# Kernel tuning notes

Measured on AMD Instinct MI355X. Metric: run time of the kernel, lower is better.

The kernel has to match this reference:

```python
import jax, jax.numpy as jnp
import numpy as np

N, E, F, H = 50000, 500000, 128, 128   # nodes, edges, in-features, hidden
L, R, B = 3, 8, 30                     # layers, relations, bases
G, C = 16, 8                           # graphs in batch, classes
EPS = 1e-5


def setup_inputs() -> dict:
    key = jax.random.key(0)
    ks = jax.random.split(key, 16)
    x = jax.random.normal(ks[0], (N, F), jnp.float32)
    edge_index = jax.random.randint(ks[1], (2, E), 0, N)
    edge_attr = jax.random.randint(ks[2], (E,), 0, R)
    batch = jnp.sort(jax.random.randint(ks[3], (N,), 0, G))
    # RGCN params (all layers share shapes since F == H)
    basis = jax.random.normal(ks[4], (L, B, H, H), jnp.float32) * 0.05
    comp = jax.random.normal(ks[5], (L, R, B), jnp.float32) * 0.2
    root = jax.random.normal(ks[6], (L, H, H), jnp.float32) * 0.05
    bias = jnp.zeros((L, H), jnp.float32)
    # BatchNorm (eval mode: running stats)
    bn1_gamma = jnp.ones((F,), jnp.float32)
    bn1_beta = jnp.zeros((F,), jnp.float32)
    bn1_mean = jax.random.normal(ks[7], (F,), jnp.float32) * 0.1
    bn1_var = jax.random.uniform(ks[8], (F,), jnp.float32, 0.5, 1.5)
    bn2_gamma = jnp.ones((H,), jnp.float32)
    bn2_beta = jnp.zeros((H,), jnp.float32)
    bn2_mean = jax.random.normal(ks[9], (H,), jnp.float32) * 0.1
    bn2_var = jax.random.uniform(ks[10], (H,), jnp.float32, 0.5, 1.5)
    fc1_w = jax.random.normal(ks[11], (H, H), jnp.float32) * 0.05
    fc1_b = jnp.zeros((H,), jnp.float32)
    fc2_w = jax.random.normal(ks[12], (H, C), jnp.float32) * 0.05
    fc2_b = jnp.zeros((C,), jnp.float32)
    return dict(x=x, edge_index=edge_index, edge_attr=edge_attr, batch=batch,
                bn1_gamma=bn1_gamma, bn1_beta=bn1_beta, bn1_mean=bn1_mean, bn1_var=bn1_var,
                basis=basis, comp=comp, root=root, bias=bias,
                bn2_gamma=bn2_gamma, bn2_beta=bn2_beta, bn2_mean=bn2_mean, bn2_var=bn2_var,
                fc1_w=fc1_w, fc1_b=fc1_b, fc2_w=fc2_w, fc2_b=fc2_b)


def _bn(x, gamma, beta, mean, var):
    return (x - mean) * jax.lax.rsqrt(var + EPS) * gamma + beta


def _rgcn_layer(x, basis_l, comp_l, root_l, bias_l, src, dst, edge_attr):
    # root transform + bias
    out = x @ root_l + bias_l
    # relation-wise basis-decomposed message passing, mean-aggregated per relation
    for r in range(R):
        W_r = jnp.einsum('b,bio->io', comp_l[r], basis_l)  # [H, H]
        xw = x @ W_r                                       # [N, H]
        mask = (edge_attr == r).astype(x.dtype)            # [E]
        msg = xw[src] * mask[:, None]                      # gather + mask
        agg = jax.ops.segment_sum(msg, dst, num_segments=N)
        deg = jax.ops.segment_sum(mask, dst, num_segments=N)
        out = out + agg / jnp.maximum(deg, 1.0)[:, None]
    return out


def reference(x, edge_index, edge_attr, batch,
              bn1_gamma, bn1_beta, bn1_mean, bn1_var,
              basis, comp, root, bias,
              bn2_gamma, bn2_beta, bn2_mean, bn2_var,
              fc1_w, fc1_b, fc2_w, fc2_b):
    src, dst = edge_index[0], edge_index[1]
    h = _bn(x, bn1_gamma, bn1_beta, bn1_mean, bn1_var)
    for l in range(L):
        h = jax.nn.relu(_rgcn_layer(h, basis[l], comp[l], root[l], bias[l], src, dst, edge_attr))
        # dropout is identity in eval mode
    # global mean pool per graph
    sums = jax.ops.segment_sum(h, batch, num_segments=G)            # [G, H]
    counts = jax.ops.segment_sum(jnp.ones((N,), h.dtype), batch, num_segments=G)
    g = sums / jnp.maximum(counts, 1.0)[:, None]
    g = _bn(g, bn2_gamma, bn2_beta, bn2_mean, bn2_var)
    # temporal_type == 'mean'
    v = jax.nn.relu(g.mean(axis=0))                                 # [H]
    v = jax.nn.relu(v @ fc1_w + fc1_b)
    logits = v @ fc2_w + fc2_b                                      # [C]
    return jax.nn.log_softmax(logits, axis=-1)
```

## Files before the change

### kernel.cpp

```cpp
#include <hip/hip_runtime.h>
#include <hip/hip_bf16.h>

#define NN 50000
#define NE 500000
#define HID 128
#define LAYERS 3
#define RELS 8
#define BASES 30
#define GRAPHS 16
#define CLASSES 8
#define EPSV 1e-5f
#define NOUT (HID * (RELS + 1))
#define SCAN_CHUNK 1024
#define SCAN_NBLK ((NN + SCAN_CHUNK - 1) / SCAN_CHUNK)
#define PCHUNK 128

typedef __attribute__((ext_vector_type(8))) short short8;
typedef __attribute__((ext_vector_type(4))) float f32x4;
typedef __attribute__((ext_vector_type(2))) float f32x2;

__device__ __forceinline__ float bf2f(unsigned short u) {
    union { unsigned int i; float f; } x; x.i = ((unsigned int)u) << 16; return x.f;
}
__device__ __forceinline__ unsigned short f2bf(float f) {
    __hip_bfloat16 b = __float2bfloat16(f);
    return *(unsigned short*)&b;
}
__device__ __forceinline__ unsigned char f2fp8(float a) {
    return (unsigned char)(__builtin_amdgcn_cvt_pk_fp8_f32(a, a, 0, false) & 0xFF);
}
__device__ __forceinline__ f32x2 fp8x2_2f(unsigned short u) {
    return __builtin_amdgcn_cvt_pk_f32_fp8((int)u, false);
}

__global__ __launch_bounds__(256) void build_wcat(const float* __restrict__ basis,
                                                  const float* __restrict__ comp,
                                                  const float* __restrict__ root,
                                                  unsigned short* __restrict__ wT) {
    int bid = blockIdx.x;
    int l = bid >> 6;
    int k0 = (bid & 63) << 1;
    __shared__ float cl[RELS * BASES];
    int tid = threadIdx.x;
    if (tid < RELS * BASES) cl[tid] = comp[l * RELS * BASES + tid];
    __syncthreads();
    int j = tid & 127;
    int k = k0 + (tid >> 7);
    const float* bp = basis + ((size_t)l * BASES * HID + k) * HID + j;
    float acc[RELS];
#pragma unroll
    for (int r = 0; r < RELS; ++r) acc[r] = 0.f;
    for (int b = 0; b < BASES; ++b) {
        float v = bp[(size_t)b * HID * HID];
#pragma unroll
        for (int r = 0; r < RELS; ++r) acc[r] += cl[r * BASES + b] * v;
    }
    unsigned short* wl = wT + (size_t)l * NOUT * HID;
#pragma unroll
    for (int r = 0; r < RELS; ++r)
        wl[(size_t)((1 + r) * HID + j) * HID + k] = f2bf(acc[r]);
    wl[(size_t)j * HID + k] = f2bf(root[((size_t)l * HID + k) * HID + j]);
}

__global__ void bn1_kernel(const float* __restrict__ x, const float* __restrict__ gamma,
                           const float* __restrict__ beta, const float* __restrict__ mean,
                           const float* __restrict__ var, unsigned short* __restrict__ habf) {
    int idx = blockIdx.x * blockDim.x + threadIdx.x;
    if (idx >= NN * HID) return;
    int f = idx & (HID - 1);
    habf[idx] = f2bf((x[idx] - mean[f]) * rsqrtf(var[f] + EPSV) * gamma[f] + beta[f]);
}

__global__ void deg_kernel(const int* __restrict__ ei, const int* __restrict__ ea,
                           float* __restrict__ deg) {
    int e = blockIdx.x * blockDim.x + threadIdx.x;
    if (e >= NE) return;
    int dst = ei[NE + e];
    atomicAdd(&deg[(size_t)dst * RELS + ea[e]], 1.0f);
}

__global__ void invdeg_kernel(float* __restrict__ deg, int* __restrict__ degi) {
    int n = blockIdx.x * blockDim.x + threadIdx.x;
    if (n >= NN) return;
    float s = 0.f;
#pragma unroll
    for (int r = 0; r < RELS; ++r) {
        float d = deg[(size_t)n * RELS + r];
        s += d;
        deg[(size_t)n * RELS + r] = 1.0f / fmaxf(d, 1.0f);
    }
    degi[n] = (int)(s + 0.5f);
}

__global__ __launch_bounds__(256) void scan_partial(const int* __restrict__ degi,
                                                    int* __restrict__ rowptr,
                                                    int* __restrict__ bsum) {
    __shared__ int ssc[256];
    int t = threadIdx.x;
    int base = blockIdx.x * SCAN_CHUNK + t * 4;
    int v[4];
#pragma unroll
    for (int j = 0; j < 4; ++j) v[j] = (base + j < NN) ? degi[base + j] : 0;
    int tsum = v[0] + v[1] + v[2] + v[3];
    ssc[t] = tsum;
    __syncthreads();
    for (int ofs = 1; ofs < 256; ofs <<= 1) {
        int add = (t >= ofs) ? ssc[t - ofs] : 0;
        __syncthreads();
        ssc[t] += add;
        __syncthreads();
    }
    int excl = ssc[t] - tsum;
    int e = 0;
#pragma unroll
    for (int j = 0; j < 4; ++j) {
        if (base + j < NN) rowptr[base + j] = excl + e;
        e += v[j];
    }
    if (t == 255) bsum[blockIdx.x] = ssc[255];
}

__global__ void scan_bsum(int* __restrict__ bsum) {
    if (threadIdx.x == 0) {
        int acc = 0;
        for (int b = 0; b < SCAN_NBLK; ++b) { int v = bsum[b]; bsum[b] = acc; acc += v; }
    }
}

__global__ __launch_bounds__(256) void scan_add(int* __restrict__ rowptr,
                                                const int* __restrict__ bsum) {
    int i = blockIdx.x * blockDim.x + threadIdx.x;
    if (i < NN) rowptr[i] += bsum[i >> 10];
    if (i == 0) rowptr[NN] = NE;
}

__global__ void fill_kernel(const int* __restrict__ ei, const int* __restrict__ ea,
                            const int* __restrict__ rowptr, const float* __restrict__ invdeg,
                            int* __restrict__ fillcnt, int* __restrict__ epk,
                            float* __restrict__ escale) {
    int e = blockIdx.x * blockDim.x + threadIdx.x;
    if (e >= NE) return;
    int src = ei[e];
    int dst = ei[NE + e];
    int r = ea[e];
    int pos = atomicAdd(&fillcnt[dst], 1);
    int slot = rowptr[dst] + pos;
    epk[slot] = src | (r << 20);
    escale[slot] = invdeg[(size_t)dst * RELS + r];
}

__global__ __launch_bounds__(256) void gemm_mfma(const unsigned short* __restrict__ habf,
                                                 const unsigned short* __restrict__ wT,
                                                 const float* __restrict__ bias,
                                                 unsigned short* __restrict__ hnb,
                                                 unsigned char* __restrict__ xwb) {
    __shared__ __align__(16) unsigned short As[64][136];
    __shared__ __align__(16) unsigned short Bs[128][72];
    int tid = threadIdx.x;
    int wave = tid >> 6, lane = tid & 63;
    int wm = (wave & 1) * 32, wn = (wave >> 1) * 64;
    int quad = lane >> 4, l16 = lane & 15;
    int row0 = blockIdx.x * 64;

    {
        int r = tid >> 2;
        int c0 = (tid & 3) * 32;
        int grow = row0 + r;
        const uint4* ga = (const uint4*)(habf + (size_t)grow * HID + c0);
        uint4 z = {0u, 0u, 0u, 0u};
#pragma unroll
        for (int c = 0; c < 4; ++c)
            *(uint4*)&As[r][c0 + c * 8] = (grow < NN) ? ga[c] : z;
    }

    for (int n0 = 0; n0 < RELS + 1; ++n0) {
        f32x4 acc[2][4];
#pragma unroll
        for (int i = 0; i < 2; ++i)
#pragma unroll
            for (int j = 0; j < 4; ++j) acc[i][j] = (f32x4){0.f, 0.f, 0.f, 0.f};

#pragma unroll
        for (int kh = 0; kh < 2; ++kh) {
            __syncthreads();
            {
                int r = tid >> 1;
                int c0 = (tid & 1) * 32;
                const uint4* gb = (const uint4*)(wT + (size_t)(n0 * 128 + r) * HID + kh * 64 + c0);
#pragma unroll
                for (int c = 0; c < 4; ++c)
                    *(uint4*)&Bs[r][c0 + c * 8] = gb[c];
            }
            __syncthreads();
#pragma unroll
            for (int kc = 0; kc < 2; ++kc) {
                int ko = kc * 32 + quad * 8;
                short8 a[2], b[4];
                a[0] = *(const short8*)&As[wm + l16][kh * 64 + ko];
                a[1] = *(const short8*)&As[wm + 16 + l16][kh * 64 + ko];
#pragma unroll
                for (int j = 0; j < 4; ++j)
                    b[j] = *(const short8*)&Bs[wn + j * 16 + l16][ko];
#pragma unroll
                for (int i = 0; i < 2; ++i)
#pragma unroll
                    for (int j = 0; j < 4; ++j)
                        acc[i][j] = __builtin_amdgcn_mfma_f32_16x16x32_bf16(a[i], b[j], acc[i][j], 0, 0, 0);
            }
        }

        if (n0 == 0) {
#pragma unroll
            for (int i = 0; i < 2; ++i)
#pragma unroll
                for (int reg = 0; reg < 4; ++reg) {
                    int grow = row0 + wm + i * 16 + quad * 4 + reg;
                    if (grow >= NN) continue;
#pragma unroll
                    for (int j = 0; j < 4; ++j) {
                        int col = wn + j * 16 + l16;
                        hnb[(size_t)grow * HID + col] = f2bf(acc[i][j][reg] + bias[col]);
                    }
                }
        } else {
            int cbase = (n0 - 1) * 128;
#pragma unroll
            for (int i = 0; i < 2; ++i)
#pragma unroll
                for (int reg = 0; reg < 4; ++reg) {
                    int grow = row0 + wm + i * 16 + quad * 4 + reg;
                    if (grow >= NN) continue;
#pragma unroll
                    for (int j = 0; j < 4; ++j) {
                        int col = wn + j * 16 + l16;
                        xwb[(size_t)grow * (RELS * HID) + cbase + col] = f2fp8(acc[i][j][reg]);
                    }
                }
        }
    }
}

__global__ __launch_bounds__(256) void aggregate_kernel(const int* __restrict__ rowptr,
                                                        const int* __restrict__ epk,
                                                        const float* __restrict__ escale,
                                                        const unsigned char* __restrict__ xwb,
                                                        const unsigned short* __restrict__ hnb,
                                                        unsigned short* __restrict__ habf) {
    int node = (blockIdx.x << 2) + (threadIdx.x >> 6);
    if (node >= NN) return;
    int lane = threadIdx.x & 63;
    int beg = rowptr[node], end = rowptr[node + 1];
    float ax = 0.f, ay = 0.f;
    for (int b0 = beg; b0 < end; b0 += 64) {
        int cnt = min(64, end - b0);
        int myp = 0; float mys = 0.f;
        if (lane < cnt) { myp = epk[b0 + lane]; mys = escale[b0 + lane]; }
        int j = 0;
        for (; j + 4 <= cnt; j += 4) {
            int p0 = __shfl(myp, j),     p1 = __shfl(myp, j + 1);
            int p2 = __shfl(myp, j + 2), p3 = __shfl(myp, j + 3);
            float s0 = __shfl(mys, j),     s1 = __shfl(mys, j + 1);
            float s2 = __shfl(mys, j + 2), s3 = __shfl(mys, j + 3);
            unsigned short u0 = *(const unsigned short*)(xwb + (size_t)(p0 & 0xFFFFF) * (RELS * HID) + (p0 >> 20) * HID + lane * 2);
            unsigned short u1 = *(const unsigned short*)(xwb + (size_t)(p1 & 0xFFFFF) * (RELS * HID) + (p1 >> 20) * HID + lane * 2);
            unsigned short u2 = *(const unsigned short*)(xwb + (size_t)(p2 & 0xFFFFF) * (RELS * HID) + (p2 >> 20) * HID + lane * 2);
            unsigned short u3 = *(const unsigned short*)(xwb + (size_t)(p3 & 0xFFFFF) * (RELS * HID) + (p3 >> 20) * HID + lane * 2);
            f32x2 v0 = fp8x2_2f(u0), v1 = fp8x2_2f(u1), v2 = fp8x2_2f(u2), v3 = fp8x2_2f(u3);
            ax += v0.x * s0 + v1.x * s1 + v2.x * s2 + v3.x * s3;
            ay += v0.y * s0 + v1.y * s1 + v2.y * s2 + v3.y * s3;
        }
        for (; j < cnt; ++j) {
            int p = __shfl(myp, j);
            float s = __shfl(mys, j);
            unsigned short u = *(const unsigned short*)(xwb + (size_t)(p & 0xFFFFF) * (RELS * HID) + (p >> 20) * HID + lane * 2);
            f32x2 v = fp8x2_2f(u);
            ax += v.x * s;
            ay += v.y * s;
        }
    }
    ushort2 cu = *((const ushort2*)(hnb + (size_t)node * HID) + lane);
    ushort2 o;
    o.x = f2bf(fmaxf(bf2f(cu.x) + ax, 0.f));
    o.y = f2bf(fmaxf(bf2f(cu.y) + ay, 0.f));
    *((ushort2*)(habf + (size_t)node * HID) + lane) = o;
}

__global__ __launch_bounds__(256) void pool_kernel(const unsigned short* __restrict__ habf,
                                                   const int* __restrict__ batch,
                                                   float* __restrict__ psum,
                                                   float* __restrict__ pcnt) {
    int tid = threadIdx.x;
    int f = tid & 127;
    int sub = tid >> 7;
    int base = blockIdx.x * PCHUNK;
    float acc = 0.f, cnt = 0.f;
    int gcur = -1;
    for (int it = 0; it < PCHUNK / 2; ++it) {
        int node = base + it * 2 + sub;
        if (node >= NN) break;
        int g = batch[node];
        if (g != gcur) {
            if (gcur >= 0) {
                atomicAdd(&psum[gcur * HID + f], acc);
                if (f == 0) atomicAdd(&pcnt[gcur], cnt);
            }
            gcur = g; acc = 0.f; cnt = 0.f;
        }
        acc += bf2f(habf[(size_t)node * HID + f]);
        cnt += 1.f;
    }
    if (gcur >= 0) {
        atomicAdd(&psum[gcur * HID + f], acc);
        if (f == 0) atomicAdd(&pcnt[gcur], cnt);
    }
}

__global__ void head_kernel(const float* __restrict__ psum, const float* __restrict__ pcnt,
                            const float* __restrict__ g2, const float* __restrict__ b2,
                            const float* __restrict__ m2, const float* __restrict__ v2,
                            const float* __restrict__ fc1w, const float* __restrict__ fc1b,
                            const float* __restrict__ fc2w, const float* __restrict__ fc2b,
                            float* __restrict__ out) {
    __shared__ float v[HID];
    __shared__ float u[HID];
    __shared__ float lg[CLASSES];
    int j = threadIdx.x;
    float acc = 0.f;
    for (int g = 0; g < GRAPHS; ++g) {
        float val = psum[g * HID + j] / fmaxf(pcnt[g], 1.0f);
        val = (val - m2[j]) * rsqrtf(v2[j] + EPSV) * g2[j] + b2[j];
        acc += val;
    }
    v[j] = fmaxf(acc / (float)GRAPHS, 0.f);
    __syncthreads();
    float s = fc1b[j];
    for (int k = 0; k < HID; ++k) s += v[k] * fc1w[k * HID + j];
    u[j] = fmaxf(s, 0.f);
    __syncthreads();
    if (j < CLASSES) {
        float t = fc2b[j];
        for (int k = 0; k < HID; ++k) t += u[k] * fc2w[k * CLASSES + j];
        lg[j] = t;
    }
    __syncthreads();
    if (j < CLASSES) {
        float mx = lg[0];
        for (int c = 1; c < CLASSES; ++c) mx = fmaxf(mx, lg[c]);
        float se = 0.f;
        for (int c = 0; c < CLASSES; ++c) se += expf(lg[c] - mx);
        out[j] = lg[j] - mx - logf(se);
    }
}

extern "C" void kernel_launch(void* const* d_in, const int* in_sizes, int n_in,
                              void* d_out, int out_size, void* d_ws, size_t ws_size,
                              hipStream_t stream) {
    const float* x     = (const float*)d_in[0];
    const int*   ei    = (const int*)d_in[1];
    const int*   ea    = (const int*)d_in[2];
    const int*   batch = (const int*)d_in[3];
    const float* bn1g  = (const float*)d_in[4];
    const float* bn1b  = (const float*)d_in[5];
    const float* bn1m  = (const float*)d_in[6];
    const float* bn1v  = (const float*)d_in[7];
    const float* basis = (const float*)d_in[8];
    const float* comp  = (const float*)d_in[9];
    const float* root  = (const float*)d_in[10];
    const float* bias  = (const float*)d_in[11];
    const float* bn2g  = (const float*)d_in[12];
    const float* bn2b  = (const float*)d_in[13];
    const float* bn2m  = (const float*)d_in[14];
    const float* bn2v  = (const float*)d_in[15];
    const float* fc1w  = (const float*)d_in[16];
    const float* fc1b  = (const float*)d_in[17];
    const float* fc2w  = (const float*)d_in[18];
    const float* fc2b  = (const float*)d_in[19];

    float* ws = (float*)d_ws;
    size_t off = 0;
    unsigned short* wT = (unsigned short*)(ws + off); off += (size_t)LAYERS * NOUT * HID / 2;
    unsigned short* hnb  = (unsigned short*)(ws + off); off += (size_t)NN * HID / 2;
    unsigned short* habf = (unsigned short*)(ws + off); off += (size_t)NN * HID / 2;
    float* deg    = ws + off; off += (size_t)NN * RELS;
    float* psum   = ws + off; off += (size_t)GRAPHS * HID + GRAPHS;
    float* pcnt   = psum + GRAPHS * HID;
    float* escale = ws + off; off += (size_t)NE;
    int* degi     = (int*)(ws + off); off += (size_t)NN;
    int* rowptr   = (int*)(ws + off); off += (size_t)NN + 1;
    int* fillcnt  = (int*)(ws + off); off += (size_t)NN;
    int* bsum     = (int*)(ws + off); off += (size_t)SCAN_NBLK;
    int* epk      = (int*)(ws + off); off += (size_t)NE;
    off = (off + 3) & ~(size_t)3;
    unsigned char* xwb = (unsigned char*)(ws + off);
    off += (size_t)NN * RELS * HID / 4;
    if (ws_size < off * sizeof(float)) return;

    hipMemsetAsync(psum, 0, (GRAPHS * HID + GRAPHS) * sizeof(float), stream);
    hipMemsetAsync(deg, 0, (size_t)NN * RELS * sizeof(float), stream);
    hipMemsetAsync(fillcnt, 0, (size_t)NN * sizeof(int), stream);

    build_wcat<<<LAYERS * 64, 256, 0, stream>>>(basis, comp, root, wT);
    bn1_kernel<<<(NN * HID + 255) / 256, 256, 0, stream>>>(x, bn1g, bn1b, bn1m, bn1v, habf);

    deg_kernel<<<(NE + 255) / 256, 256, 0, stream>>>(ei, ea, deg);
    invdeg_kernel<<<(NN + 255) / 256, 256, 0, stream>>>(deg, degi);
    scan_partial<<<SCAN_NBLK, 256, 0, stream>>>(degi, rowptr, bsum);
    scan_bsum<<<1, 64, 0, stream>>>(bsum);
    scan_add<<<(NN + 255) / 256, 256, 0, stream>>>(rowptr, bsum);
    fill_kernel<<<(NE + 255) / 256, 256, 0, stream>>>(ei, ea, rowptr, deg, fillcnt, epk, escale);

    for (int l = 0; l < LAYERS; ++l) {
        gemm_mfma<<<(NN + 63) / 64, 256, 0, stream>>>(habf, wT + (size_t)l * NOUT * HID,
                                                      bias + (size_t)l * HID, hnb, xwb);
        aggregate_kernel<<<(NN + 3) / 4, 256, 0, stream>>>(rowptr, epk, escale, xwb, hnb, habf);
    }

    pool_kernel<<<(NN + PCHUNK - 1) / PCHUNK, 256, 0, stream>>>(habf, batch, psum, pcnt);
    head_kernel<<<1, 128, 0, stream>>>(psum, pcnt, bn2g, bn2b, bn2m, bn2v,
                                       fc1w, fc1b, fc2w, fc2b, (float*)d_out);
}
```

Baseline: 451.2 us.

## Transpose MFMA operands for packed GEMM stores and XOR-swizzle shared tiles

Swaps the A and B operands of the MFMA so each lane's accumulator holds four consecutive output columns of one row. This lets the epilogue write packed 8-byte bf16 and 4-byte fp8 stores instead of scattered single-element stores. The padded shared-memory tiles are replaced with unpadded tiles that use an XOR swizzle to avoid LDS bank conflicts while saving shared memory. The risks are the correctness of the swizzle indexing and the less coalesced per-lane row addressing in the stores.

```diff
diff --git a/kernel.cpp b/kernel.cpp
--- a/kernel.cpp
+++ b/kernel.cpp
@@ -25,9 +25,6 @@
 __device__ __forceinline__ unsigned short f2bf(float f) {
     __hip_bfloat16 b = __float2bfloat16(f);
     return *(unsigned short*)&b;
-}
-__device__ __forceinline__ unsigned char f2fp8(float a) {
-    return (unsigned char)(__builtin_amdgcn_cvt_pk_fp8_f32(a, a, 0, false) & 0xFF);
 }
 __device__ __forceinline__ f32x2 fp8x2_2f(unsigned short u) {
     return __builtin_amdgcn_cvt_pk_f32_fp8((int)u, false);
@@ -154,23 +151,26 @@
                                                  const float* __restrict__ bias,
                                                  unsigned short* __restrict__ hnb,
                                                  unsigned char* __restrict__ xwb) {
-    __shared__ __align__(16) unsigned short As[64][136];
-    __shared__ __align__(16) unsigned short Bs[128][72];
+    __shared__ __align__(16) unsigned short As[64][128];
+    __shared__ __align__(16) unsigned short Bs[128][64];
     int tid = threadIdx.x;
     int wave = tid >> 6, lane = tid & 63;
-    int wm = (wave & 1) * 32, wn = (wave >> 1) * 64;
+    int wm = (wave & 1) * 32;
+    int wn = (wave >> 1) * 64;
     int quad = lane >> 4, l16 = lane & 15;
     int row0 = blockIdx.x * 64;
 
     {
         int r = tid >> 2;
-        int c0 = (tid & 3) * 32;
+        int u0 = (tid & 3) * 4;
         int grow = row0 + r;
-        const uint4* ga = (const uint4*)(habf + (size_t)grow * HID + c0);
+        const uint4* ga = (const uint4*)(habf + (size_t)grow * HID + u0 * 8);
         uint4 z = {0u, 0u, 0u, 0u};
 #pragma unroll
-        for (int c = 0; c < 4; ++c)
-            *(uint4*)&As[r][c0 + c * 8] = (grow < NN) ? ga[c] : z;
+        for (int q = 0; q < 4; ++q) {
+            int pu = (u0 + q) ^ (r & 7);
+            *(uint4*)&As[r][pu << 3] = (grow < NN) ? ga[q] : z;
+        }
     }
 
     for (int n0 = 0; n0 < RELS + 1; ++n0) {
@@ -185,57 +185,68 @@
             __syncthreads();
             {
                 int r = tid >> 1;
-                int c0 = (tid & 1) * 32;
-                const uint4* gb = (const uint4*)(wT + (size_t)(n0 * 128 + r) * HID + kh * 64 + c0);
-#pragma unroll
-                for (int c = 0; c < 4; ++c)
-                    *(uint4*)&Bs[r][c0 + c * 8] = gb[c];
+                int u0 = (tid & 1) * 4;
+                const uint4* gb = (const uint4*)(wT + (size_t)(n0 * 128 + r) * HID + kh * 64 + u0 * 8);
+#pragma unroll
+                for (int q = 0; q < 4; ++q) {
+                    int pu = (u0 + q) ^ (r & 7);
+                    *(uint4*)&Bs[r][pu << 3] = gb[q];
+                }
             }
             __syncthreads();
 #pragma unroll
             for (int kc = 0; kc < 2; ++kc) {
-                int ko = kc * 32 + quad * 8;
-                short8 a[2], b[4];
-                a[0] = *(const short8*)&As[wm + l16][kh * 64 + ko];
-                a[1] = *(const short8*)&As[wm + 16 + l16][kh * 64 + ko];
-#pragma unroll
-                for (int j = 0; j < 4; ++j)
-                    b[j] = *(const short8*)&Bs[wn + j * 16 + l16][ko];
+                short8 aop[4], bop[2];
+#pragma unroll
+                for (int j = 0; j < 4; ++j) {
+                    int fr = wn + j * 16 + l16;
+                    int pu = (kc * 4 + quad) ^ (l16 & 7);
+                    aop[j] = *(const short8*)&Bs[fr][pu << 3];
+                }
+#pragma unroll
+                for (int i = 0; i < 2; ++i) {
+                    int sr = wm + i * 16 + l16;
+                    int pu = (kh * 8 + kc * 4 + quad) ^ (l16 & 7);
+                    bop[i] = *(const short8*)&As[sr][pu << 3];
+                }
 #pragma unroll
                 for (int i = 0; i < 2; ++i)
 #pragma unroll
                     for (int j = 0; j < 4; ++j)
-                        acc[i][j] = __builtin_amdgcn_mfma_f32_16x16x32_bf16(a[i], b[j], acc[i][j], 0, 0, 0);
+                        acc[i][j] = __builtin_amdgcn_mfma_f32_16x16x32_bf16(aop[j], bop[i], acc[i][j], 0, 0, 0);
             }
         }
 
         if (n0 == 0) {
 #pragma unroll
-            for (int i = 0; i < 2; ++i)
-#pragma unroll
-                for (int reg = 0; reg < 4; ++reg) {
-                    int grow = row0 + wm + i * 16 + quad * 4 + reg;
-                    if (grow >= NN) continue;
-#pragma unroll
-                    for (int j = 0; j < 4; ++j) {
-                        int col = wn + j * 16 + l16;
-                        hnb[(size_t)grow * HID + col] = f2bf(acc[i][j][reg] + bias[col]);
-                    }
+            for (int i = 0; i < 2; ++i) {
+                int src = row0 + wm + i * 16 + l16;
+                if (src >= NN) continue;
+#pragma unroll
+                for (int j = 0; j < 4; ++j) {
+                    int f0 = wn + j * 16 + quad * 4;
+                    unsigned lo = (unsigned)f2bf(acc[i][j][0] + bias[f0 + 0]) |
+                                  ((unsigned)f2bf(acc[i][j][1] + bias[f0 + 1]) << 16);
+                    unsigned hi = (unsigned)f2bf(acc[i][j][2] + bias[f0 + 2]) |
+                                  ((unsigned)f2bf(acc[i][j][3] + bias[f0 + 3]) << 16);
+                    uint2 pk = {lo, hi};
+                    *(uint2*)(hnb + (size_t)src * HID + f0) = pk;
                 }
+            }
         } else {
             int cbase = (n0 - 1) * 128;
 #pragma unroll
-            for (int i = 0; i < 2; ++i)
-#pragma unroll
-                for (int reg = 0; reg < 4; ++reg) {
-                    int grow = row0 + wm + i * 16 + quad * 4 + reg;
-                    if (grow >= NN) continue;
-#pragma unroll
-                    for (int j = 0; j < 4; ++j) {
-                        int col = wn + j * 16 + l16;
-                        xwb[(size_t)grow * (RELS * HID) + cbase + col] = f2fp8(acc[i][j][reg]);
-                    }
+            for (int i = 0; i < 2; ++i) {
+                int src = row0 + wm + i * 16 + l16;
+                if (src >= NN) continue;
+#pragma unroll
+                for (int j = 0; j < 4; ++j) {
+                    int f0 = wn + j * 16 + quad * 4;
+                    unsigned w = (unsigned)__builtin_amdgcn_cvt_pk_fp8_f32(acc[i][j][0], acc[i][j][1], 0, false);
+                    w = (unsigned)__builtin_amdgcn_cvt_pk_fp8_f32(acc[i][j][2], acc[i][j][3], (int)w, true);
+                    *(unsigned*)(xwb + (size_t)src * (RELS * HID) + cbase + f0) = w;
                 }
+            }
         }
     }
 }
```

Measured after the change: 492.8 us. 1.09x slower.

## Retile GEMM to 128x128 blocks with 2D grid over output chunks

Applied to the files above, without the earlier changes.

The GEMM kernel no longer has each block loop over all nine output column chunks. It now launches a 2D grid where each block computes one 128-row by 128-column tile, and each wave holds a 64x64 register accumulator (4x4 MFMA tiles) instead of 32x64. This raises parallelism and the MFMA-to-LDS-load ratio per wave. In exchange, each A row tile is now reloaded from global memory for every column chunk, and register pressure per thread goes up.

```diff
diff --git a/kernel.cpp b/kernel.cpp
--- a/kernel.cpp
+++ b/kernel.cpp
@@ -154,89 +154,79 @@
                                                  const float* __restrict__ bias,
                                                  unsigned short* __restrict__ hnb,
                                                  unsigned char* __restrict__ xwb) {
-    __shared__ __align__(16) unsigned short As[64][136];
+    __shared__ __align__(16) unsigned short As[128][72];
     __shared__ __align__(16) unsigned short Bs[128][72];
     int tid = threadIdx.x;
     int wave = tid >> 6, lane = tid & 63;
-    int wm = (wave & 1) * 32, wn = (wave >> 1) * 64;
+    int wm = (wave & 1) * 64, wn = (wave >> 1) * 64;
     int quad = lane >> 4, l16 = lane & 15;
-    int row0 = blockIdx.x * 64;
-
-    {
-        int r = tid >> 2;
-        int c0 = (tid & 3) * 32;
-        int grow = row0 + r;
-        const uint4* ga = (const uint4*)(habf + (size_t)grow * HID + c0);
+    int row0 = blockIdx.x * 128;
+    int n0 = blockIdx.y;
+
+    f32x4 acc[4][4];
+#pragma unroll
+    for (int i = 0; i < 4; ++i)
+#pragma unroll
+        for (int j = 0; j < 4; ++j) acc[i][j] = (f32x4){0.f, 0.f, 0.f, 0.f};
+
+    int srow = tid >> 1;
+    int shalf = (tid & 1) * 32;
+    for (int k0 = 0; k0 < HID; k0 += 64) {
+        int grow = row0 + srow;
+        const uint4* ga = (const uint4*)(habf + (size_t)grow * HID + k0 + shalf);
+        const uint4* gb = (const uint4*)(wT + (size_t)(n0 * 128 + srow) * HID + k0 + shalf);
         uint4 z = {0u, 0u, 0u, 0u};
 #pragma unroll
-        for (int c = 0; c < 4; ++c)
-            *(uint4*)&As[r][c0 + c * 8] = (grow < NN) ? ga[c] : z;
-    }
-
-    for (int n0 = 0; n0 < RELS + 1; ++n0) {
-        f32x4 acc[2][4];
-#pragma unroll
-        for (int i = 0; i < 2; ++i)
-#pragma unroll
-            for (int j = 0; j < 4; ++j) acc[i][j] = (f32x4){0.f, 0.f, 0.f, 0.f};
-
-#pragma unroll
-        for (int kh = 0; kh < 2; ++kh) {
-            __syncthreads();
-            {
-                int r = tid >> 1;
-                int c0 = (tid & 1) * 32;
-                const uint4* gb = (const uint4*)(wT + (size_t)(n0 * 128 + r) * HID + kh * 64 + c0);
-#pragma unroll
-                for (int c = 0; c < 4; ++c)
-                    *(uint4*)&Bs[r][c0 + c * 8] = gb[c];
+        for (int c = 0; c < 4; ++c) {
+            *(uint4*)&As[srow][shalf + c * 8] = (grow < NN) ? ga[c] : z;
+            *(uint4*)&Bs[srow][shalf + c * 8] = gb[c];
+        }
+        __syncthreads();
+#pragma unroll
+        for (int kc = 0; kc < 2; ++kc) {
+            int ko = kc * 32 + quad * 8;
+            short8 a[4], b[4];
+#pragma unroll
+            for (int i = 0; i < 4; ++i) {
+                a[i] = *(const short8*)&As[wm + i * 16 + l16][ko];
+                b[i] = *(const short8*)&Bs[wn + i * 16 + l16][ko];
             }
-            __syncthreads();
-#pragma unroll
-            for (int kc = 0; kc < 2; ++kc) {
-                int ko = kc * 32 + quad * 8;
-                short8 a[2], b[4];
-                a[0] = *(const short8*)&As[wm + l16][kh * 64 + ko];
-                a[1] = *(const short8*)&As[wm + 16 + l16][kh * 64 + ko];
+#pragma unroll
+            for (int i = 0; i < 4; ++i)
 #pragma unroll
                 for (int j = 0; j < 4; ++j)
-                    b[j] = *(const short8*)&Bs[wn + j * 16 + l16][ko];
-#pragma unroll
-                for (int i = 0; i < 2; ++i)
-#pragma unroll
-                    for (int j = 0; j < 4; ++j)
-                        acc[i][j] = __builtin_amdgcn_mfma_f32_16x16x32_bf16(a[i], b[j], acc[i][j], 0, 0, 0);
+                    acc[i][j] = __builtin_amdgcn_mfma_f32_16x16x32_bf16(a[i], b[j], acc[i][j], 0, 0, 0);
+        }
+        __syncthreads();
+    }
+
+    if (n0 == 0) {
+#pragma unroll
+        for (int i = 0; i < 4; ++i)
+#pragma unroll
+            for (int reg = 0; reg < 4; ++reg) {
+                int grow = row0 + wm + i * 16 + quad * 4 + reg;
+                if (grow >= NN) continue;
+#pragma unroll
+                for (int j = 0; j < 4; ++j) {
+                    int col = wn + j * 16 + l16;
+                    hnb[(size_t)grow * HID + col] = f2bf(acc[i][j][reg] + bias[col]);
+                }
             }
-        }
-
-        if (n0 == 0) {
-#pragma unroll
-            for (int i = 0; i < 2; ++i)
-#pragma unroll
-                for (int reg = 0; reg < 4; ++reg) {
-                    int grow = row0 + wm + i * 16 + quad * 4 + reg;
-                    if (grow >= NN) continue;
-#pragma unroll
-                    for (int j = 0; j < 4; ++j) {
-                        int col = wn + j * 16 + l16;
-                        hnb[(size_t)grow * HID + col] = f2bf(acc[i][j][reg] + bias[col]);
-                    }
+    } else {
+        int cbase = (n0 - 1) * 128;
+#pragma unroll
+        for (int i = 0; i < 4; ++i)
+#pragma unroll
+            for (int reg = 0; reg < 4; ++reg) {
+                int grow = row0 + wm + i * 16 + quad * 4 + reg;
+                if (grow >= NN) continue;
+#pragma unroll
+                for (int j = 0; j < 4; ++j) {
+                    int col = wn + j * 16 + l16;
+                    xwb[(size_t)grow * (RELS * HID) + cbase + col] = f2fp8(acc[i][j][reg]);
                 }
-        } else {
-            int cbase = (n0 - 1) * 128;
-#pragma unroll
-            for (int i = 0; i < 2; ++i)
-#pragma unroll
-                for (int reg = 0; reg < 4; ++reg) {
-                    int grow = row0 + wm + i * 16 + quad * 4 + reg;
-                    if (grow >= NN) continue;
-#pragma unroll
-                    for (int j = 0; j < 4; ++j) {
-                        int col = wn + j * 16 + l16;
-                        xwb[(size_t)grow * (RELS * HID) + cbase + col] = f2fp8(acc[i][j][reg]);
-                    }
-                }
-        }
+            }
     }
 }
 
@@ -409,9 +399,10 @@
     scan_add<<<(NN + 255) / 256, 256, 0, stream>>>(rowptr, bsum);
     fill_kernel<<<(NE + 255) / 256, 256, 0, stream>>>(ei, ea, rowptr, deg, fillcnt, epk, escale);
 
+    dim3 ggrid((NN + 127) / 128, RELS + 1);
     for (int l = 0; l < LAYERS; ++l) {
-        gemm_mfma<<<(NN + 63) / 64, 256, 0, stream>>>(habf, wT + (size_t)l * NOUT * HID,
-                                                      bias + (size_t)l * HID, hnb, xwb);
+        gemm_mfma<<<ggrid, 256, 0, stream>>>(habf, wT + (size_t)l * NOUT * HID,
+                                             bias + (size_t)l * HID, hnb, xwb);
         aggregate_kernel<<<(NN + 3) / 4, 256, 0, stream>>>(rowptr, epk, escale, xwb, hnb, habf);
     }
 
```

Measured after the change: 467.7 us. +3.7%, slower.
